# Kernel tuning notes

Measured on AMD Instinct MI355X. Metric: run time of the kernel, lower is better.

The kernel has to match this reference:

```python
import jax, jax.numpy as jnp
import numpy as np

N_NODES = 50000
N_EDGES = 1600000
D = 128


def setup_inputs() -> dict:
    key = jax.random.key(0)
    ks = jax.random.split(key, 8)
    features = jax.random.normal(ks[0], (N_NODES, D), dtype=jnp.float32)
    edge_src = jax.random.randint(ks[1], (N_EDGES,), 0, N_NODES, dtype=jnp.int32)
    edge_dst = jax.random.randint(ks[2], (N_EDGES,), 0, N_NODES, dtype=jnp.int32)
    edge_weight = jax.random.uniform(ks[3], (N_EDGES,), dtype=jnp.float32)
    scale = 1.0 / np.sqrt(D)
    W1 = jax.random.normal(ks[4], (D, D), dtype=jnp.float32) * scale
    b1 = jnp.zeros((D,), dtype=jnp.float32)
    W2 = jax.random.normal(ks[5], (D, D), dtype=jnp.float32) * scale
    b2 = jnp.zeros((D,), dtype=jnp.float32)
    return {"features": features, "edge_src": edge_src, "edge_dst": edge_dst,
            "edge_weight": edge_weight, "W1": W1, "b1": b1, "W2": W2, "b2": b2}


def _gcn_layer(x, W, b, edge_src, edge_dst, edge_weight, n_nodes):
    # support = X @ W  (dense projection), then spmm: out[d] += w_e * support[s]
    support = x @ W  # [N, D]
    msgs = support[edge_src] * edge_weight[:, None]  # [E, D] gather + scale
    out = jax.ops.segment_sum(msgs, edge_dst, num_segments=n_nodes)  # scatter-add
    return out + b


def reference(features, edge_src, edge_dst, edge_weight, W1, b1, W2, b2):
    h = _gcn_layer(features, W1, b1, edge_src, edge_dst, edge_weight, N_NODES)
    h = jax.nn.relu(h)
    # dropout is identity in eval mode (training=False)
    out = _gcn_layer(h, W2, b2, edge_src, edge_dst, edge_weight, N_NODES)
    return out
```

## Files before the change

kernel.cpp:

```cpp
#include <hip/hip_runtime.h>
#include <hip/hip_fp16.h>

#define D 128
#define BSHIFT 7
#define BSIZE (1 << BSHIFT)
#define CHUNK 8192
#define CAP 6400
#define LDP 136
#define SENTV 0xFFFFFFFFu

typedef _Float16 half8 __attribute__((ext_vector_type(8)));
typedef float f32x4 __attribute__((ext_vector_type(4)));

__global__ __launch_bounds__(512) void init_bcur(int* __restrict__ bcur, int NB) {
    const int b = blockIdx.x * 512 + threadIdx.x;
    if (b < NB) bcur[b] = b * CAP;
}

__device__ __forceinline__ void gemm_body_f32(const float* __restrict__ X,
                                              const __half* __restrict__ Wt,
                                              __half* __restrict__ Y, int M, int bx) {
    const int lane = threadIdx.x & 63;
    const int wv = threadIdx.x >> 6;
    const int row0 = bx * 64 + wv * 16;
    const int m = lane & 15;
    const int q = lane >> 4;

    const int rsafe = min(row0 + m, M - 1);
    const float4* Xr = (const float4*)(X + (size_t)rsafe * D);
    half8 a[4];
#pragma unroll
    for (int kt = 0; kt < 4; ++kt) {
        const float4 lo = Xr[kt * 8 + q * 2];
        const float4 hi = Xr[kt * 8 + q * 2 + 1];
        a[kt] = (half8){(_Float16)lo.x, (_Float16)lo.y, (_Float16)lo.z,
                        (_Float16)lo.w, (_Float16)hi.x, (_Float16)hi.y,
                        (_Float16)hi.z, (_Float16)hi.w};
    }

    const half8* WT8 = (const half8*)Wt;
#pragma unroll
    for (int ct = 0; ct < 8; ++ct) {
        const int n = ct * 16 + m;
        f32x4 acc = {0.f, 0.f, 0.f, 0.f};
#pragma unroll
        for (int kt = 0; kt < 4; ++kt) {
            const half8 b = WT8[(size_t)n * 16 + kt * 4 + q];
            acc = __builtin_amdgcn_mfma_f32_16x16x32_f16(a[kt], b, acc, 0, 0, 0);
        }
#pragma unroll
        for (int r = 0; r < 4; ++r) {
            const int orow = row0 + q * 4 + r;
            if (orow < M)
                Y[(size_t)orow * D + ct * 16 + m] = __float2half(acc[r]);
        }
    }
}

__global__ __launch_bounds__(256) void scatter_prep(const int* __restrict__ src,
                                                    const int* __restrict__ dst,
                                                    const float* __restrict__ wgt,
                                                    int* __restrict__ bcur,
                                                    unsigned int* __restrict__ csrA,
                                                    int E, int NB, int nscat,
                                                    const float* __restrict__ W1,
                                                    const float* __restrict__ W2,
                                                    __half* __restrict__ W1t,
                                                    __half* __restrict__ W2t) {
    if (blockIdx.x >= (unsigned)nscat) {
        const int which = blockIdx.x - nscat;
        const float* W = which ? W2 : W1;
        __half* Wt = which ? W2t : W1t;
        for (int i = threadIdx.x; i < D * D; i += 256) {
            const int n = i >> 7, k = i & 127;
            Wt[i] = __float2half(W[k * D + n]);
        }
        return;
    }

    __shared__ int lhist[512];
    __shared__ int lstart[512];
    __shared__ int lcur[512];
    const int tid = threadIdx.x;
    const int base = blockIdx.x * CHUNK;

    for (int b = tid; b < NB; b += 256) lhist[b] = 0;
    __syncthreads();

    int dreg[CHUNK / 256];
#pragma unroll
    for (int u = 0; u < CHUNK / 256; ++u) {
        const int e = base + u * 256 + tid;
        dreg[u] = (e < E) ? dst[e] : -1;
        if (dreg[u] >= 0) atomicAdd(&lhist[dreg[u] >> BSHIFT], 1);
    }
    __syncthreads();

    for (int b = tid; b < NB; b += 256) {
        const int c = lhist[b];
        if (c) {
            const int r = atomicAdd(&bcur[b], (c + 15) & ~15);
            lstart[b] = r;
            lcur[b] = r;
        }
    }
    __syncthreads();

#pragma unroll
    for (int u = 0; u < CHUNK / 256; ++u) {
        const int d = dreg[u];
        if (d >= 0) {
            const int e = base + u * 256 + tid;
            const int b = d >> BSHIFT;
            const int pos = atomicAdd(&lcur[b], 1);
            const unsigned int wq =
                (unsigned int)__float2int_rn(wgt[e] * 511.0f);
            const unsigned int kv = (unsigned int)src[e] |
                                    ((unsigned int)(d & (BSIZE - 1)) << 16) |
                                    (wq << 23);
            if (pos < (b + 1) * CAP) csrA[pos] = kv;
        }
    }
    __syncthreads();

    for (int b = tid; b < NB; b += 256) {
        const int c = lhist[b];
        if (c) {
            const int beg = lstart[b] + c;
            const int fin = lstart[b] + ((c + 15) & ~15);
            for (int p = beg; p < fin; ++p)
                if (p < (b + 1) * CAP) csrA[p] = SENTV;
        }
    }
}

__global__ __launch_bounds__(256) void sort_gemm1(const unsigned int* __restrict__ csrA,
                                                  const int* __restrict__ bcur,
                                                  int* __restrict__ offsets,
                                                  int* __restrict__ deg,
                                                  unsigned int* __restrict__ csr,
                                                  int M, int NB,
                                                  const float* __restrict__ X,
                                                  const __half* __restrict__ W1t,
                                                  __half* __restrict__ sup) {
    if (blockIdx.x >= (unsigned)NB) {
        gemm_body_f32(X, W1t, sup, M, blockIdx.x - NB);
        return;
    }

    __shared__ int hist[BSIZE];
    __shared__ int ncur[BSIZE];
    __shared__ int wtot[2];
    const int b = blockIdx.x;
    const int n0 = b << BSHIFT;
    const int tid = threadIdx.x;
    const int nloc = min(BSIZE, M - n0);
    const int bstart = b * CAP;
    const int bend = min(bcur[b], (b + 1) * CAP);

    if (tid < BSIZE) hist[tid] = 0;
    __syncthreads();

    unsigned int reg[CAP / 256];
#pragma unroll
    for (int i = 0; i < CAP / 256; ++i) {
        const int j = bstart + i * 256 + tid;
        unsigned int kv = SENTV;
        if (j < bend) kv = csrA[j];
        reg[i] = kv;
        if ((kv & 0xFFFFu) != 0xFFFFu)
            atomicAdd(&hist[(kv >> 16) & (BSIZE - 1)], 1);
    }
    __syncthreads();

    const int lane = tid & 63;
    const int wv = tid >> 6;
    const int v = (tid < BSIZE) ? hist[tid] : 0;
    int incl = v;
#pragma unroll
    for (int off = 1; off < 64; off <<= 1) {
        int t = __shfl_up(incl, off, 64);
        if (lane >= off) incl += t;
    }
    if (tid < BSIZE && lane == 63) wtot[wv] = incl;
    __syncthreads();
    const int carry = (wv == 1) ? wtot[0] : 0;
    const int excl = bstart + incl - v + carry;
    if (tid < nloc) {
        offsets[n0 + tid] = excl;
        deg[n0 + tid] = v;
        ncur[tid] = excl;
    }
    __syncthreads();

#pragma unroll
    for (int i = 0; i < CAP / 256; ++i) {
        const unsigned int kv = reg[i];
        if ((kv & 0xFFFFu) != 0xFFFFu) {
            const int pos = atomicAdd(&ncur[(kv >> 16) & (BSIZE - 1)], 1);
            csr[pos] = kv;
        }
    }
}

__device__ __forceinline__ void accum8(float acc[8], float4 raw, float w) {
    const __half2* h = (const __half2*)&raw;
#pragma unroll
    for (int i = 0; i < 4; ++i) {
        const float2 f = __half22float2(h[i]);
        acc[2 * i]     = fmaf(w, f.x, acc[2 * i]);
        acc[2 * i + 1] = fmaf(w, f.y, acc[2 * i + 1]);
    }
}

__device__ __forceinline__ float kv_w(unsigned int kv) {
    return (float)(kv >> 23) * (1.0f / 511.0f);
}

__device__ __forceinline__ void gather_row(const float4* __restrict__ sup4,
                                           const unsigned int* __restrict__ csr,
                                           int beg, int end, int l, float acc[8]) {
    int j = beg;
    for (; j + 8 <= end; j += 8) {
        unsigned int kv[8];
        float4 r[8];
#pragma unroll
        for (int u = 0; u < 8; ++u) kv[u] = csr[j + u];
#pragma unroll
        for (int u = 0; u < 8; ++u)
            r[u] = sup4[(size_t)(kv[u] & 0xFFFF) * 16 + l];
#pragma unroll
        for (int u = 0; u < 8; ++u) accum8(acc, r[u], kv_w(kv[u]));
    }
    if (j + 4 <= end) {
        unsigned int kv[4];
        float4 r[4];
#pragma unroll
        for (int u = 0; u < 4; ++u) kv[u] = csr[j + u];
#pragma unroll
        for (int u = 0; u < 4; ++u)
            r[u] = sup4[(size_t)(kv[u] & 0xFFFF) * 16 + l];
#pragma unroll
        for (int u = 0; u < 4; ++u) accum8(acc, r[u], kv_w(kv[u]));
        j += 4;
    }
    for (; j < end; ++j) {
        const unsigned int kv = csr[j];
        const float4 r = sup4[(size_t)(kv & 0xFFFF) * 16 + l];
        accum8(acc, r, kv_w(kv));
    }
}

__global__ __launch_bounds__(256) void gather_gemm(const __half* __restrict__ sup,
                                                   const int* __restrict__ offsets,
                                                   const int* __restrict__ deg,
                                                   const unsigned int* __restrict__ csr,
                                                   const float* __restrict__ b1,
                                                   const __half* __restrict__ W2t,
                                                   __half* __restrict__ sup2, int M) {
    __shared__ _Float16 hA[16 * LDP];
    const int tid = threadIdx.x;
    const int q = tid >> 4;
    const int l = tid & 15;
    const int n = blockIdx.x * 16 + q;

    float acc[8];
    {
        const float4 c0 = ((const float4*)b1)[l * 2];
        const float4 c1 = ((const float4*)b1)[l * 2 + 1];
        acc[0] = c0.x; acc[1] = c0.y; acc[2] = c0.z; acc[3] = c0.w;
        acc[4] = c1.x; acc[5] = c1.y; acc[6] = c1.z; acc[7] = c1.w;
    }
    if (n < M) {
        const int beg = offsets[n];
        gather_row((const float4*)sup, csr, beg, beg + deg[n], l, acc);
    }

    half8 hv;
#pragma unroll
    for (int i = 0; i < 8; ++i) hv[i] = (_Float16)fmaxf(acc[i], 0.f);
    *(half8*)&hA[q * LDP + l * 8] = hv;
    __syncthreads();

    const int lane = tid & 63;
    const int wv = tid >> 6;
    const int m = lane & 15;
    const int qq = lane >> 4;
    half8 a[4];
#pragma unroll
    for (int kt = 0; kt < 4; ++kt)
        a[kt] = *(const half8*)&hA[m * LDP + kt * 32 + qq * 8];

    const half8* WT8 = (const half8*)W2t;
#pragma unroll
    for (int c = 0; c < 2; ++c) {
        const int ct = wv * 2 + c;
        const int ncol = ct * 16 + m;
        f32x4 dacc = {0.f, 0.f, 0.f, 0.f};
#pragma unroll
        for (int kt = 0; kt < 4; ++kt) {
            const half8 b = WT8[(size_t)ncol * 16 + kt * 4 + qq];
            dacc = __builtin_amdgcn_mfma_f32_16x16x32_f16(a[kt], b, dacc, 0, 0, 0);
        }
#pragma unroll
        for (int r = 0; r < 4; ++r) {
            const int orow = blockIdx.x * 16 + qq * 4 + r;
            if (orow < M)
                sup2[(size_t)orow * D + ct * 16 + m] = __float2half(dacc[r]);
        }
    }
}

__global__ __launch_bounds__(256) void gather_out(const __half* __restrict__ sup,
                                                  const int* __restrict__ offsets,
                                                  const int* __restrict__ deg,
                                                  const unsigned int* __restrict__ csr,
                                                  const float* __restrict__ bias,
                                                  float* __restrict__ out, int M) {
    const int tid = threadIdx.x;
    const int q = tid >> 4;
    const int l = tid & 15;
    const int n = blockIdx.x * 16 + q;
    if (n >= M) return;

    float acc[8];
    {
        const float4 c0 = ((const float4*)bias)[l * 2];
        const float4 c1 = ((const float4*)bias)[l * 2 + 1];
        acc[0] = c0.x; acc[1] = c0.y; acc[2] = c0.z; acc[3] = c0.w;
        acc[4] = c1.x; acc[5] = c1.y; acc[6] = c1.z; acc[7] = c1.w;
    }
    const int beg = offsets[n];
    gather_row((const float4*)sup, csr, beg, beg + deg[n], l, acc);

    f32x4* out4 = (f32x4*)out;
    const f32x4 o0 = {acc[0], acc[1], acc[2], acc[3]};
    const f32x4 o1 = {acc[4], acc[5], acc[6], acc[7]};
    __builtin_nontemporal_store(o0, out4 + (size_t)n * 32 + l * 2);
    __builtin_nontemporal_store(o1, out4 + (size_t)n * 32 + l * 2 + 1);
}

extern "C" void kernel_launch(void* const* d_in, const int* in_sizes, int n_in,
                              void* d_out, int out_size, void* d_ws, size_t ws_size,
                              hipStream_t stream) {
    const float* features = (const float*)d_in[0];
    const int*   esrc     = (const int*)d_in[1];
    const int*   edst     = (const int*)d_in[2];
    const float* ew       = (const float*)d_in[3];
    const float* W1       = (const float*)d_in[4];
    const float* b1       = (const float*)d_in[5];
    const float* W2       = (const float*)d_in[6];
    const float* b2       = (const float*)d_in[7];
    float* out = (float*)d_out;

    const int M = in_sizes[0] / D;
    const int E = in_sizes[1];
    const int NB = (M + BSIZE - 1) >> BSHIFT;

    unsigned int* csrA = (unsigned int*)d_ws;
    unsigned int* csr  = csrA + (size_t)NB * CAP;
    __half* sup     = (__half*)(csr + (size_t)NB * CAP);
    __half* sup2    = sup + (size_t)M * D;
    int*    offsets = (int*)(sup2 + (size_t)M * D);
    int*    deg     = offsets + M;
    int*    bcur    = deg + M;
    __half* W1t     = (__half*)(bcur + NB);
    __half* W2t     = W1t + D * D;

    const int gemm_blocks = (M + 63) / 64;
    const int node_blocks = (M + 15) / 16;
    const int nscat = (E + CHUNK - 1) / CHUNK;

    init_bcur<<<1, 512, 0, stream>>>(bcur, NB);
    scatter_prep<<<nscat + 2, 256, 0, stream>>>(esrc, edst, ew, bcur, csrA, E, NB,
                                                nscat, W1, W2, W1t, W2t);
    sort_gemm1<<<NB + gemm_blocks, 256, 0, stream>>>(csrA, bcur, offsets, deg, csr,
                                                     M, NB, features, W1t, sup);
    gather_gemm<<<node_blocks, 256, 0, stream>>>(sup, offsets, deg, csr, b1, W2t,
                                                 sup2, M);
    gather_out<<<node_blocks, 256, 0, stream>>>(sup2, offsets, deg, csr, b2, out, M);
}
```

Measured before the change: 256.3 us.

## Sub-bin edges by source range and gather chunks in lockstep for cache locality

```diff
diff --git a/kernel.cpp b/kernel.cpp
--- a/kernel.cpp
+++ b/kernel.cpp
@@ -8,6 +8,9 @@
 #define CAP 6400
 #define LDP 136
 #define SENTV 0xFFFFFFFFu
+#define SUBB 8
+#define SSH 13
+#define NBIN (BSIZE * SUBB)
 
 typedef _Float16 half8 __attribute__((ext_vector_type(8)));
 typedef float f32x4 __attribute__((ext_vector_type(4)));
@@ -136,8 +139,7 @@
 
 __global__ __launch_bounds__(256) void sort_gemm1(const unsigned int* __restrict__ csrA,
                                                   const int* __restrict__ bcur,
-                                                  int* __restrict__ offsets,
-                                                  int* __restrict__ deg,
+                                                  int* __restrict__ boff,
                                                   unsigned int* __restrict__ csr,
                                                   int M, int NB,
                                                   const float* __restrict__ X,
@@ -148,9 +150,9 @@
         return;
     }
 
-    __shared__ int hist[BSIZE];
-    __shared__ int ncur[BSIZE];
-    __shared__ int wtot[2];
+    __shared__ int hist[NBIN];
+    __shared__ int binoff[NBIN];
+    __shared__ int wtot[4];
     const int b = blockIdx.x;
     const int n0 = b << BSHIFT;
     const int tid = threadIdx.x;
@@ -158,7 +160,7 @@
     const int bstart = b * CAP;
     const int bend = min(bcur[b], (b + 1) * CAP);
 
-    if (tid < BSIZE) hist[tid] = 0;
+    for (int i = tid; i < NBIN; i += 256) hist[i] = 0;
     __syncthreads();
 
     unsigned int reg[CAP / 256];
@@ -168,36 +170,47 @@
         unsigned int kv = SENTV;
         if (j < bend) kv = csrA[j];
         reg[i] = kv;
-        if ((kv & 0xFFFFu) != 0xFFFFu)
-            atomicAdd(&hist[(kv >> 16) & (BSIZE - 1)], 1);
-    }
-    __syncthreads();
-
+        if ((kv & 0xFFFFu) != 0xFFFFu) {
+            const int key = (int)(((kv >> 16) & (BSIZE - 1)) << 3) |
+                            (int)((kv & 0xFFFFu) >> SSH);
+            atomicAdd(&hist[key], 1);
+        }
+    }
+    __syncthreads();
+
+    int loc[4];
+    int run = 0;
+#pragma unroll
+    for (int k = 0; k < 4; ++k) { loc[k] = run; run += hist[tid * 4 + k]; }
     const int lane = tid & 63;
     const int wv = tid >> 6;
-    const int v = (tid < BSIZE) ? hist[tid] : 0;
-    int incl = v;
+    int incl = run;
 #pragma unroll
     for (int off = 1; off < 64; off <<= 1) {
-        int t = __shfl_up(incl, off, 64);
+        const int t = __shfl_up(incl, off, 64);
         if (lane >= off) incl += t;
     }
-    if (tid < BSIZE && lane == 63) wtot[wv] = incl;
-    __syncthreads();
-    const int carry = (wv == 1) ? wtot[0] : 0;
-    const int excl = bstart + incl - v + carry;
-    if (tid < nloc) {
-        offsets[n0 + tid] = excl;
-        deg[n0 + tid] = v;
-        ncur[tid] = excl;
-    }
+    if (lane == 63) wtot[wv] = incl;
+    __syncthreads();
+    int carry = 0;
+#pragma unroll
+    for (int w = 0; w < 3; ++w)
+        if (w < wv) carry += wtot[w];
+    const int base = bstart + carry + incl - run;
+#pragma unroll
+    for (int k = 0; k < 4; ++k) binoff[tid * 4 + k] = base + loc[k];
+    __syncthreads();
+
+    for (int i = tid; i < nloc * SUBB; i += 256) boff[n0 * SUBB + i] = binoff[i];
     __syncthreads();
 
 #pragma unroll
     for (int i = 0; i < CAP / 256; ++i) {
         const unsigned int kv = reg[i];
         if ((kv & 0xFFFFu) != 0xFFFFu) {
-            const int pos = atomicAdd(&ncur[(kv >> 16) & (BSIZE - 1)], 1);
+            const int key = (int)(((kv >> 16) & (BSIZE - 1)) << 3) |
+                            (int)((kv & 0xFFFFu) >> SSH);
+            const int pos = atomicAdd(&binoff[key], 1);
             csr[pos] = kv;
         }
     }
@@ -251,9 +264,21 @@
     }
 }
 
+__device__ __forceinline__ void load_chunks(const int* __restrict__ boff, int n,
+                                            bool act, int st[8]) {
+    if (act) {
+        const int4 s0 = ((const int4*)boff)[(size_t)n * 2];
+        const int4 s1 = ((const int4*)boff)[(size_t)n * 2 + 1];
+        st[0] = s0.x; st[1] = s0.y; st[2] = s0.z; st[3] = s0.w;
+        st[4] = s1.x; st[5] = s1.y; st[6] = s1.z; st[7] = s1.w;
+    } else {
+#pragma unroll
+        for (int k = 0; k < 8; ++k) st[k] = 0;
+    }
+}
+
 __global__ __launch_bounds__(256) void gather_gemm(const __half* __restrict__ sup,
-                                                   const int* __restrict__ offsets,
-                                                   const int* __restrict__ deg,
+                                                   const int* __restrict__ boff,
                                                    const unsigned int* __restrict__ csr,
                                                    const float* __restrict__ b1,
                                                    const __half* __restrict__ W2t,
@@ -263,6 +288,7 @@
     const int q = tid >> 4;
     const int l = tid & 15;
     const int n = blockIdx.x * 16 + q;
+    const bool act = (n < M);
 
     float acc[8];
     {
@@ -271,9 +297,14 @@
         acc[0] = c0.x; acc[1] = c0.y; acc[2] = c0.z; acc[3] = c0.w;
         acc[4] = c1.x; acc[5] = c1.y; acc[6] = c1.z; acc[7] = c1.w;
     }
-    if (n < M) {
-        const int beg = offsets[n];
-        gather_row((const float4*)sup, csr, beg, beg + deg[n], l, acc);
+    int st[8];
+    load_chunks(boff, n, act, st);
+    const float4* sup4 = (const float4*)sup;
+
+#pragma unroll
+    for (int c = 0; c < 7; ++c) {
+        gather_row(sup4, csr, st[c], st[c + 1], l, acc);
+        if (c < 6) __syncthreads();
     }
 
     half8 hv;
@@ -312,8 +343,7 @@
 }
 
 __global__ __launch_bounds__(256) void gather_out(const __half* __restrict__ sup,
-                                                  const int* __restrict__ offsets,
-                                                  const int* __restrict__ deg,
+                                                  const int* __restrict__ boff,
                                                   const unsigned int* __restrict__ csr,
                                                   const float* __restrict__ bias,
                                                   float* __restrict__ out, int M) {
@@ -321,7 +351,7 @@
     const int q = tid >> 4;
     const int l = tid & 15;
     const int n = blockIdx.x * 16 + q;
-    if (n >= M) return;
+    const bool act = (n < M);
 
     float acc[8];
     {
@@ -330,14 +360,23 @@
         acc[0] = c0.x; acc[1] = c0.y; acc[2] = c0.z; acc[3] = c0.w;
         acc[4] = c1.x; acc[5] = c1.y; acc[6] = c1.z; acc[7] = c1.w;
     }
-    const int beg = offsets[n];
-    gather_row((const float4*)sup, csr, beg, beg + deg[n], l, acc);
-
-    f32x4* out4 = (f32x4*)out;
-    const f32x4 o0 = {acc[0], acc[1], acc[2], acc[3]};
-    const f32x4 o1 = {acc[4], acc[5], acc[6], acc[7]};
-    __builtin_nontemporal_store(o0, out4 + (size_t)n * 32 + l * 2);
-    __builtin_nontemporal_store(o1, out4 + (size_t)n * 32 + l * 2 + 1);
+    int st[8];
+    load_chunks(boff, n, act, st);
+    const float4* sup4 = (const float4*)sup;
+
+#pragma unroll
+    for (int c = 0; c < 7; ++c) {
+        gather_row(sup4, csr, st[c], st[c + 1], l, acc);
+        if (c < 6) __syncthreads();
+    }
+
+    if (act) {
+        f32x4* out4 = (f32x4*)out;
+        const f32x4 o0 = {acc[0], acc[1], acc[2], acc[3]};
+        const f32x4 o1 = {acc[4], acc[5], acc[6], acc[7]};
+        __builtin_nontemporal_store(o0, out4 + (size_t)n * 32 + l * 2);
+        __builtin_nontemporal_store(o1, out4 + (size_t)n * 32 + l * 2 + 1);
+    }
 }
 
 extern "C" void kernel_launch(void* const* d_in, const int* in_sizes, int n_in,
@@ -361,9 +400,8 @@
     unsigned int* csr  = csrA + (size_t)NB * CAP;
     __half* sup     = (__half*)(csr + (size_t)NB * CAP);
     __half* sup2    = sup + (size_t)M * D;
-    int*    offsets = (int*)(sup2 + (size_t)M * D);
-    int*    deg     = offsets + M;
-    int*    bcur    = deg + M;
+    int*    boff    = (int*)(sup2 + (size_t)M * D);
+    int*    bcur    = boff + (size_t)M * SUBB;
     __half* W1t     = (__half*)(bcur + NB);
     __half* W2t     = W1t + D * D;
 
@@ -374,9 +412,8 @@
     init_bcur<<<1, 512, 0, stream>>>(bcur, NB);
     scatter_prep<<<nscat + 2, 256, 0, stream>>>(esrc, edst, ew, bcur, csrA, E, NB,
                                                 nscat, W1, W2, W1t, W2t);
-    sort_gemm1<<<NB + gemm_blocks, 256, 0, stream>>>(csrA, bcur, offsets, deg, csr,
+    sort_gemm1<<<NB + gemm_blocks, 256, 0, stream>>>(csrA, bcur, boff, csr,
                                                      M, NB, features, W1t, sup);
-    gather_gemm<<<node_blocks, 256, 0, stream>>>(sup, offsets, deg, csr, b1, W2t,
-                                                 sup2, M);
-    gather_out<<<node_blocks, 256, 0, stream>>>(sup2, offsets, deg, csr, b2, out, M);
-}
+    gather_gemm<<<node_blocks, 256, 0, stream>>>(sup, boff, csr, b1, W2t, sup2, M);
+    gather_out<<<node_blocks, 256, 0, stream>>>(sup2, boff, csr, b2, out, M);
+}
```

After: 334.7 us. +30.6%, slower.
